# Optimization experiments

Measured on AMD Instinct MI355X. Metric: run time of the kernel, lower is better.

Reference implementation:

```python
import jax, jax.numpy as jnp
import numpy as np
from jax import lax

D_MODEL = 128
D_INNER = 256   # expand * d_model
D_STATE = 16
D_CONV = 4
DT_RANK = 8     # ceil(d_model / 16)
IN_CH = 64
SCALE = 0.02


def setup_inputs() -> dict:
    key = jax.random.key(0)
    ks = jax.random.split(key, 16)
    r = lambda k, s: jax.random.normal(k, s, dtype=jnp.float32)
    return {
        "x": r(ks[0], (4, IN_CH, 128, 128)),
        "conv_w": r(ks[1], (D_MODEL, IN_CH, 3, 3)) * SCALE,
        "conv_b": r(ks[2], (D_MODEL,)) * SCALE,
        "bn_g": jnp.ones((D_MODEL,), jnp.float32),
        "bn_b": jnp.zeros((D_MODEL,), jnp.float32),
        "bn_mean": r(ks[3], (D_MODEL,)) * SCALE,
        "bn_var": jax.random.uniform(ks[4], (D_MODEL,), jnp.float32) + 0.5,
        "in_w": r(ks[5], (2 * D_INNER, D_MODEL)) * SCALE,
        "conv1d_w": r(ks[6], (D_INNER, 1, D_CONV)) * SCALE,
        "conv1d_b": r(ks[7], (D_INNER,)) * SCALE,
        "xproj_w": r(ks[8], (DT_RANK + 2 * D_STATE, D_INNER)) * SCALE,
        "dtproj_w": r(ks[9], (D_INNER, DT_RANK)) * SCALE,
        "dtproj_b": r(ks[10], (D_INNER,)) * SCALE,
        "A_log": r(ks[11], (D_INNER, D_STATE)) * 0.5,
        "Dp": r(ks[12], (D_INNER,)) * SCALE,
        "out_w": r(ks[13], (D_MODEL, D_INNER)) * SCALE,
    }


def _mamba(u, in_w, conv1d_w, conv1d_b, xproj_w, dtproj_w, dtproj_b, A_log, Dp, out_w):
    # u: [B, L, d_model]
    xz = jnp.einsum("bld,ed->ble", u, in_w)          # [B, L, 2*d_inner]
    x_in, z = jnp.split(xz, 2, axis=-1)
    # depthwise causal conv1d over L
    xc = lax.conv_general_dilated(
        x_in.transpose(0, 2, 1), conv1d_w, (1,), [(D_CONV - 1, 0)],
        dimension_numbers=("NCL", "OIL", "NCL"), feature_group_count=D_INNER,
    ) + conv1d_b[None, :, None]
    x_in = jax.nn.silu(xc).transpose(0, 2, 1)         # [B, L, d_inner]

    x_dbl = jnp.einsum("bld,ed->ble", x_in, xproj_w)  # [B, L, dt_rank+2*d_state]
    dt, Bm, Cm = jnp.split(x_dbl, [DT_RANK, DT_RANK + D_STATE], axis=-1)
    delta = jax.nn.softplus(jnp.einsum("blr,dr->bld", dt, dtproj_w) + dtproj_b)

    A = -jnp.exp(A_log)                               # [d_inner, d_state]
    deltaA = jnp.exp(jnp.einsum("bld,dn->bldn", delta, A))        # [B,L,d,n]
    deltaBu = jnp.einsum("bld,bln,bld->bldn", delta, Bm, x_in)    # [B,L,d,n]

    def step(h, inp):
        dA, dBu, c = inp                              # [B,d,n],[B,d,n],[B,n]
        h = dA * h + dBu
        y = jnp.einsum("bdn,bn->bd", h, c)
        return h, y

    Bsz, L = u.shape[0], u.shape[1]
    h0 = jnp.zeros((Bsz, D_INNER, D_STATE), u.dtype)
    _, ys = lax.scan(step, h0, (deltaA.transpose(1, 0, 2, 3),
                                deltaBu.transpose(1, 0, 2, 3),
                                Cm.transpose(1, 0, 2)))
    y = ys.transpose(1, 0, 2) + x_in * Dp             # [B, L, d_inner]
    y = y * jax.nn.silu(z)
    return jnp.einsum("bld,ed->ble", y, out_w)        # [B, L, d_model]


def reference(x, conv_w, conv_b, bn_g, bn_b, bn_mean, bn_var, in_w, conv1d_w,
              conv1d_b, xproj_w, dtproj_w, dtproj_b, A_log, Dp, out_w):
    # downsample: conv3x3 stride2 + BN(eval) + exact GELU
    y = lax.conv_general_dilated(x, conv_w, (2, 2), [(1, 1), (1, 1)],
                                 dimension_numbers=("NCHW", "OIHW", "NCHW"))
    y = y + conv_b[None, :, None, None]
    inv = bn_g / jnp.sqrt(bn_var + 1e-5)
    y = (y - bn_mean[None, :, None, None]) * inv[None, :, None, None] + bn_b[None, :, None, None]
    y = jax.nn.gelu(y, approximate=False)             # [B, C, H, W]

    B, C, H, W = y.shape
    u = y.reshape(B, C, H * W).transpose(0, 2, 1)     # [B, L, C]
    out = _mamba(u, in_w, conv1d_w, conv1d_b, xproj_w, dtproj_w, dtproj_b,
                 A_log, Dp, out_w)
    out = out.transpose(0, 2, 1).reshape(B, C, H, W)
    return y + out
```

## Files before the change

kernel.cpp:

```cpp
#include <hip/hip_runtime.h>
#include <math.h>

#define NB 4
#define LTOK 4096
#define DM 128
#define DI 256
#define NCH 256
#define TCH 16
#define GSZ 16
#define NG  16

#define OFF_A2     0u
#define OFF_BIAS2  73728u
#define OFF_YDSR   84096u
#define OFF_XPRE   2181248u
#define OFF_S0     4278400u
#define OFF_Z      6375552u
#define OFF_DELTA  10569856u
#define OFF_S1     12667008u
#define OFF_BC     14764160u
#define OFF_DSUM   15288448u
#define OFF_GS     15550592u
#define OFF_GD     15812736u
#define OFF_XT     15829120u
#define OFF_WBF    17926272u
#define OFF_WCMP   17963136u
#define OFF_DPREF  18004096u
#define OFF_INWBF  19052672u
#define OFF_OUTWBF 19085440u

#define DEV __device__ __forceinline__
#define L2E 1.4426950408889634f

typedef short bh8 __attribute__((ext_vector_type(8)));
typedef float f4v __attribute__((ext_vector_type(4)));

DEV float fast_silu(float v) {
  return v * __builtin_amdgcn_rcpf(1.f + __expf(-v));
}

DEV unsigned short f2bf(float f) {
  unsigned int u = __float_as_uint(f);
  u = (u + 0x7FFFu + ((u >> 16) & 1u)) >> 16;
  return (unsigned short)u;
}

DEV float bf2f(unsigned short us) {
  return __uint_as_float((unsigned int)us << 16);
}

DEV float upk(const unsigned int* p, int i) {
  unsigned int u = p[i >> 1];
  return __uint_as_float((i & 1) ? (u & 0xFFFF0000u) : (u << 16));
}

__global__ __launch_bounds__(256) void k0x_prep(
    const float* __restrict__ conv_w, const float* __restrict__ conv_b,
    const float* __restrict__ bn_g, const float* __restrict__ bn_b,
    const float* __restrict__ bn_mean, const float* __restrict__ bn_var,
    const float* __restrict__ xproj_w, const float* __restrict__ A_log,
    const float* __restrict__ dtw, const float* __restrict__ in_w,
    const float* __restrict__ out_w, const float* __restrict__ x,
    float* __restrict__ ws) {
  __shared__ float t[64][65];
  if (blockIdx.x >= 1009) {
    const int bid = blockIdx.x - 1009;
    unsigned short* xt = (unsigned short*)(ws + OFF_XT);
    const int tid = threadIdx.x;
    const int ixh = bid & 1;
    const int iy = (bid >> 1) & 127;
    const int b = bid >> 8;
    {
      const int ixl = tid & 63, cw = tid >> 6;
#pragma unroll 4
      for (int i = 0; i < 16; ++i) {
        int ci = cw * 16 + i;
        t[ci][ixl] = x[(((size_t)(b * 64 + ci) * 128) + iy) * 128 + ixh * 64 + ixl];
      }
    }
    __syncthreads();
    {
      const int cil = tid & 63, iw = tid >> 6;
      unsigned short* dst = xt + (((size_t)(b * 128 + iy) * 128) + ixh * 64) * 64;
#pragma unroll 4
      for (int i = 0; i < 16; ++i) {
        int ix = iw * 16 + i;
        dst[ix * 64 + cil] = f2bf(t[cil][ix]);
      }
    }
    return;
  }
  int i = blockIdx.x * 256 + threadIdx.x;
  if (i < 73728) {
    int ci = i & 63; int tap = (i >> 6) % 9; int co = i / 576;
    float inv = bn_g[co] * rsqrtf(bn_var[co] + 1e-5f);
    ((unsigned short*)(ws + OFF_WBF))[i] = f2bf(conv_w[co * 576 + ci * 9 + tap] * inv);
  } else if (i < 73856) {
    int co = i - 73728;
    float inv = bn_g[co] * rsqrtf(bn_var[co] + 1e-5f);
    ws[OFF_BIAS2 + co] = (conv_b[co] - bn_mean[co]) * inv + bn_b[co];
  } else if (i < 77952) {
    int j = i - 73856;
    ws[OFF_A2 + j] = -__expf(A_log[j]) * L2E;
  } else if (i < 159872) {
    int j = i - 77952;
    int n = j >> 8, k = j & 255;
    float v = 0.f;
    if (n < 256) {
#pragma unroll
      for (int r = 0; r < 8; ++r)
        v = fmaf(dtw[n * 8 + r], xproj_w[r * 256 + k], v);
    } else if (n < 288) {
      v = xproj_w[(8 + n - 256) * 256 + k];
    }
    ((unsigned short*)(ws + OFF_WCMP))[j] = f2bf(v);
  } else if (i < 225408) {
    int j = i - 159872;
    ((unsigned short*)(ws + OFF_INWBF))[j] = f2bf(in_w[j]);
  } else if (i < 258176) {
    int j = i - 225408;
    ((unsigned short*)(ws + OFF_OUTWBF))[j] = f2bf(out_w[j]);
  }
}

__global__ __launch_bounds__(512) void k12_conv_inproj(
    const unsigned short* __restrict__ xt, const unsigned short* __restrict__ wbf,
    const float* __restrict__ bias2, const unsigned short* __restrict__ inwbf,
    unsigned short* __restrict__ ydsr, unsigned short* __restrict__ xpre,
    unsigned short* __restrict__ z) {
  __shared__ unsigned short ldt[64][136];
  const int tid = threadIdx.x;
  const int lane = tid & 63;
  const int w = tid >> 6;
  const int col = lane & 15, quad = lane >> 4;
  const int oy = blockIdx.x & 63;
  const int b = blockIdx.x >> 6;
  const int co_w = w * 16;
  const int iy0 = 2 * oy - 1;
  const bh8 bzero = {};

  f4v acc[4];
#pragma unroll
  for (int nt = 0; nt < 4; ++nt) acc[nt] = (f4v){0.f, 0.f, 0.f, 0.f};
  const unsigned short* ap = wbf + (size_t)(co_w + col) * 576;
  for (int tap = 0; tap < 9; ++tap) {
    const int kh = tap / 3, kw = tap - kh * 3;
    const int iy = iy0 + kh;
    const unsigned short* xrow = xt + (long)(b * 128 + iy) * 8192;
    const bool oky = (iy >= 0);
#pragma unroll
    for (int kc = 0; kc < 2; ++kc) {
      const int cib = kc * 32 + quad * 8;
      bh8 a0 = *(const bh8*)&ap[tap * 64 + cib];
#pragma unroll
      for (int nt = 0; nt < 4; ++nt) {
        const int ix = 2 * (nt * 16 + col) - 1 + kw;
        bh8 bv = *(const bh8*)&xrow[(long)ix * 64 + cib];
        if (!(oky && ix >= 0)) bv = bzero;
        acc[nt] = __builtin_amdgcn_mfma_f32_16x16x32_bf16(a0, bv, acc[nt], 0, 0, 0);
      }
    }
  }
#pragma unroll
  for (int nt = 0; nt < 4; ++nt) {
    const int tok = nt * 16 + col;
    const int swz = (tok & 15) << 3;
#pragma unroll
    for (int r = 0; r < 4; ++r) {
      const int co = co_w + quad * 4 + r;
      float v = acc[nt][r] + bias2[co];
      float g = 0.5f * v * (1.f + erff(v * 0.70710678118f));
      unsigned short gb = f2bf(g);
      ydsr[(((size_t)(b * 128 + co) * 64) + oy) * 64 + tok] = gb;
      ldt[tok][co ^ swz] = gb;
    }
  }
  __syncthreads();

  const size_t tglob0 = (size_t)(b * 4096 + oy * 64);
#pragma unroll
  for (int tt = 0; tt < 4; ++tt) {
    const int row = tt * 16 + col;
    const int swz = (row & 15) << 3;
    bh8 afrag[4];
#pragma unroll
    for (int kb = 0; kb < 4; ++kb)
      afrag[kb] = *(const bh8*)&ldt[row][(quad * 8 + kb * 32) ^ swz];
    f4v acc2[4];
#pragma unroll
    for (int j = 0; j < 4; ++j) acc2[j] = (f4v){0.f, 0.f, 0.f, 0.f};
#pragma unroll
    for (int kb = 0; kb < 4; ++kb) {
#pragma unroll
      for (int j = 0; j < 4; ++j) {
        const int e_row = (w * 4 + j) * 16 + col;
        bh8 bfrag = *(const bh8*)&inwbf[(size_t)e_row * 128 + quad * 8 + kb * 32];
        acc2[j] = __builtin_amdgcn_mfma_f32_16x16x32_bf16(afrag[kb], bfrag, acc2[j], 0, 0, 0);
      }
    }
#pragma unroll
    for (int j = 0; j < 4; ++j) {
      const int e = (w * 4 + j) * 16 + col;
#pragma unroll
      for (int r = 0; r < 4; ++r) {
        const size_t t = tglob0 + tt * 16 + quad * 4 + r;
        if (e < 256) xpre[t * 256 + e] = f2bf(acc2[j][r]);
        else z[t * 256 + e - 256] = f2bf(acc2[j][r]);
      }
    }
  }
}

__global__ __launch_bounds__(256) void k45_mfma(
    const unsigned short* __restrict__ wcomp, const float* __restrict__ dtb,
    const unsigned short* __restrict__ xpre, const float* __restrict__ cw1,
    const float* __restrict__ cb1, const float* __restrict__ a2tab,
    unsigned short* __restrict__ xinbf, unsigned short* __restrict__ delta,
    float* __restrict__ bc, float* __restrict__ dsum,
    float* __restrict__ S0, float* __restrict__ S1) {
  __shared__ unsigned short ld_xin[16][264];
  __shared__ unsigned short ld_delta[16][264];
  __shared__ float ld_bc[16][33];
  const int tid = threadIdx.x;
  const int lane = tid & 63;
  const int w = tid >> 6;
  const int col = lane & 15, quad = lane >> 4;
  const int tt = blockIdx.x & 255, b = blockIdx.x >> 8;
  const int t0 = tt * 16;

  {
    const int d = tid;
    float4 w4 = *(const float4*)&cw1[d * 4];
    float bias = cb1[d];
    float xw[19];
    const unsigned short* xp = xpre + ((size_t)(b * 4096 + t0 - 3)) * 256 + d;
    if (tt > 0) {
#pragma unroll
      for (int i = 0; i < 19; ++i) xw[i] = bf2f(xp[(size_t)i * 256]);
    } else {
#pragma unroll
      for (int i = 0; i < 19; ++i) {
        int t = t0 - 3 + i;
        xw[i] = (t >= 0) ? bf2f(xp[(size_t)i * 256]) : 0.f;
      }
    }
    unsigned short* dst = xinbf + ((size_t)(b * 4096 + t0)) * 256 + d;
#pragma unroll
    for (int i = 0; i < 16; ++i) {
      float o = bias + w4.x * xw[i] + w4.y * xw[i + 1] + w4.z * xw[i + 2] +
                w4.w * xw[i + 3];
      unsigned short us = f2bf(fast_silu(o));
      ld_xin[i][d] = us;
      dst[(size_t)i * 256] = us;
    }
  }
  __syncthreads();

  {
    bh8 afrag[8];
#pragma unroll
    for (int kb = 0; kb < 8; ++kb)
      afrag[kb] = *(const bh8*)&ld_xin[col][quad * 8 + kb * 32];
    f4v acc[5];
#pragma unroll
    for (int j = 0; j < 5; ++j) acc[j] = (f4v){0.f, 0.f, 0.f, 0.f};

    const int nt0 = w * 5;
    const unsigned short* wb = wcomp + (size_t)(nt0 * 16 + col) * 256 + quad * 8;
#pragma unroll
    for (int kb = 0; kb < 8; ++kb) {
#pragma unroll
      for (int j = 0; j < 5; ++j) {
        bh8 bfrag = *(const bh8*)&wb[(size_t)j * 4096 + kb * 32];
        acc[j] = __builtin_amdgcn_mfma_f32_16x16x32_bf16(afrag[kb], bfrag, acc[j], 0, 0, 0);
      }
    }
#pragma unroll
    for (int j = 0; j < 5; ++j) {
      const int n = (nt0 + j) * 16 + col;
      if (n < 256) {
        float bias = dtb[n];
#pragma unroll
        for (int r = 0; r < 4; ++r) {
          float s = acc[j][r] + bias;
          float dl = fmaxf(s, 0.f) + __logf(1.f + __expf(-fabsf(s)));
          ld_delta[quad * 4 + r][n] = f2bf(dl);
        }
      } else if (n < 288) {
#pragma unroll
        for (int r = 0; r < 4; ++r) ld_bc[quad * 4 + r][n - 256] = acc[j][r];
      }
    }
  }
  __syncthreads();

  {
    const int d = tid;
    float A2[16];
#pragma unroll
    for (int j = 0; j < 4; ++j) {
      float4 a = *(const float4*)&a2tab[d * 16 + j * 4];
      A2[4 * j + 0] = a.x; A2[4 * j + 1] = a.y;
      A2[4 * j + 2] = a.z; A2[4 * j + 3] = a.w;
    }
    float h[16];
#pragma unroll
    for (int n = 0; n < 16; ++n) h[n] = 0.f;
    float ds = 0.f;
#pragma unroll 4
    for (int i = 0; i < TCH; ++i) {
      float dl = bf2f(ld_delta[i][d]);
      float xv = bf2f(ld_xin[i][d]);
      ds += dl;
      float dlx = dl * xv;
#pragma unroll
      for (int n = 0; n < 16; ++n)
        h[n] = fmaf(exp2f(dl * A2[n]), h[n], dlx * ld_bc[i][n]);
    }
    dsum[((size_t)b * NCH + tt) * 256 + d] = ds;
    float* S = (b & 2) ? (S1 + (size_t)(b & 1) * 1048576)
                       : (S0 + (size_t)(b & 1) * 1048576);
    const size_t sbase = ((size_t)tt * 16) * 256 + d;
#pragma unroll
    for (int n = 0; n < 16; ++n) S[sbase + (size_t)n * 256] = h[n];
  }

#pragma unroll
  for (int it = 0; it < 4; ++it) {
    int idx = it * 256 + tid;
    int row = idx >> 6, d4 = (idx & 63) * 4;
    unsigned long long pk = *(const unsigned long long*)&ld_delta[row][d4];
    *(unsigned long long*)&delta[((size_t)(b * 4096 + t0 + row)) * 256 + d4] = pk;
  }
  if (tid < 128) {
    int row = tid >> 3, q = (tid & 7) * 4;
    float4 v = make_float4(ld_bc[row][q], ld_bc[row][q + 1],
                           ld_bc[row][q + 2], ld_bc[row][q + 3]);
    *(float4*)&bc[((size_t)(b * 4096 + t0 + row)) * 32 + q] = v;
  }
}

__global__ __launch_bounds__(256) void k5b1_group(
    float* __restrict__ S0, float* __restrict__ S1,
    const float* __restrict__ dsum, const float* __restrict__ a2tab,
    float* __restrict__ Gs, float* __restrict__ Gd,
    float* __restrict__ dpref) {
  const int d = threadIdx.x;
  const int n = blockIdx.x & 15, g = (blockIdx.x >> 4) & (NG - 1),
            b = blockIdx.x >> 8;
  float* S = (b & 2) ? (S1 + (size_t)(b & 1) * 1048576)
                     : (S0 + (size_t)(b & 1) * 1048576);
  const float A2 = a2tab[d * 16 + n];
  const size_t s0 = ((size_t)(g * GSZ) * 16 + n) * 256 + d;
  const size_t d0 = ((size_t)b * NCH + g * GSZ) * 256 + d;
  float sv[GSZ], dv[GSZ];
#pragma unroll
  for (int k = 0; k < GSZ; ++k) {
    sv[k] = S[s0 + (size_t)k * 4096];
    dv[k] = dsum[d0 + (size_t)k * 256];
  }
  float h = 0.f, cum = 0.f;
#pragma unroll
  for (int k = 0; k < GSZ; ++k) {
    S[s0 + (size_t)k * 4096] = h;
    if (n == 0) dpref[d0 + (size_t)k * 256] = cum;
    h = fmaf(exp2f(A2 * dv[k]), h, sv[k]);
    cum += dv[k];
  }
  Gs[((size_t)(b * NG + g) * 16 + n) * 256 + d] = h;
  if (n == 0) Gd[((size_t)b * NG + g) * 256 + d] = cum;
}

__global__ __launch_bounds__(256) void k56_fused(
    const unsigned short* __restrict__ xinbf, const float* __restrict__ bc,
    const unsigned short* __restrict__ delta, const unsigned short* __restrict__ z,
    const float* __restrict__ a2tab, const float* __restrict__ Dp,
    const float* __restrict__ dpref, const float* __restrict__ Gs,
    const float* __restrict__ Gd,
    const float* __restrict__ S0, const float* __restrict__ S1,
    const unsigned short* __restrict__ outwbf, const unsigned short* __restrict__ ydsr,
    float* __restrict__ out) {
  __shared__ __align__(16) float bct[TCH * 32];
  __shared__ __align__(16) unsigned short ld_y[16][264];
  __shared__ float ldo[16][132];
  const int tid = threadIdx.x;
  const int d = tid;
  const int c = blockIdx.x & (NCH - 1), b = blockIdx.x >> 8;
  const int t0 = c * TCH;
  {
    const float* src = bc + (size_t)(b * 4096 + t0) * 32;
    for (int i = tid; i < TCH * 32; i += 256) bct[i] = src[i];
  }
  float A2[16];
#pragma unroll
  for (int j = 0; j < 4; ++j) {
    float4 a = *(const float4*)&a2tab[d * 16 + j * 4];
    A2[4 * j + 0] = a.x; A2[4 * j + 1] = a.y;
    A2[4 * j + 2] = a.z; A2[4 * j + 3] = a.w;
  }
  const float Dpd = Dp[d];
  const int g = c >> 4;
  const float dp0 = dpref[((size_t)b * NCH + c) * 256 + d];

  const size_t base = (size_t)(b * 4096 + t0) * 256 + d;
  unsigned int dlp[8], xvp[8], zvp[8];
  {
    const unsigned short* pd = delta + base;
    const unsigned short* px = xinbf + base;
    const unsigned short* pz = z + base;
#pragma unroll
    for (int j = 0; j < 8; ++j) {
      dlp[j] = (unsigned int)pd[(size_t)(2 * j) * 256] |
               ((unsigned int)pd[(size_t)(2 * j + 1) * 256] << 16);
      xvp[j] = (unsigned int)px[(size_t)(2 * j) * 256] |
               ((unsigned int)px[(size_t)(2 * j + 1) * 256] << 16);
      zvp[j] = (unsigned int)pz[(size_t)(2 * j) * 256] |
               ((unsigned int)pz[(size_t)(2 * j + 1) * 256] << 16);
    }
  }
  const float* S = (b & 2) ? (S1 + (size_t)(b & 1) * 1048576)
                           : (S0 + (size_t)(b & 1) * 1048576);
  const size_t sbase = ((size_t)c * 16) * 256 + d;
  float sv[16];
#pragma unroll
  for (int n = 0; n < 16; ++n) sv[n] = S[sbase + (size_t)n * 256];

  float h[16];
#pragma unroll
  for (int n = 0; n < 16; ++n) h[n] = 0.f;
#pragma unroll
  for (int gp = 0; gp < NG - 1; ++gp) {
    if (gp < g) {
      const float gdv = Gd[((size_t)b * NG + gp) * 256 + d];
      const size_t gb0 = ((size_t)(b * NG + gp) * 16) * 256 + d;
#pragma unroll
      for (int n = 0; n < 16; ++n)
        h[n] = fmaf(exp2f(A2[n] * gdv), h[n], Gs[gb0 + (size_t)n * 256]);
    }
  }
#pragma unroll
  for (int n = 0; n < 16; ++n)
    h[n] = fmaf(exp2f(A2[n] * dp0), h[n], sv[n]);
  __syncthreads();
#pragma unroll
  for (int i = 0; i < TCH; ++i) {
    float dl = upk(dlp, i);
    float xv = upk(xvp, i);
    float zv = upk(zvp, i);
    float dlx = dl * xv;
    const float* r = &bct[i * 32];
    float y = 0.f;
#pragma unroll
    for (int n = 0; n < 16; ++n) {
      h[n] = fmaf(exp2f(dl * A2[n]), h[n], dlx * r[n]);
      y = fmaf(h[n], r[16 + n], y);
    }
    ld_y[i][d] = f2bf((y + xv * Dpd) * fast_silu(zv));
  }
  __syncthreads();

  const int lane = tid & 63;
  const int w = tid >> 6;
  const int col = lane & 15, quad = lane >> 4;
  const int oy = t0 >> 6, ox0 = t0 & 63;
  bh8 afrag[8];
#pragma unroll
  for (int kb = 0; kb < 8; ++kb)
    afrag[kb] = *(const bh8*)&ld_y[col][quad * 8 + kb * 32];
  f4v acc[2];
#pragma unroll
  for (int j = 0; j < 2; ++j) acc[j] = (f4v){0.f, 0.f, 0.f, 0.f};
  const int nt0 = w * 2;
  const unsigned short* wb = outwbf + (size_t)(nt0 * 16 + col) * 256 + quad * 8;
#pragma unroll
  for (int kb = 0; kb < 8; ++kb) {
#pragma unroll
    for (int j = 0; j < 2; ++j) {
      bh8 bfrag = *(const bh8*)&wb[(size_t)j * 4096 + kb * 32];
      acc[j] = __builtin_amdgcn_mfma_f32_16x16x32_bf16(afrag[kb], bfrag, acc[j], 0, 0, 0);
    }
  }
#pragma unroll
  for (int j = 0; j < 2; ++j)
#pragma unroll
    for (int r = 0; r < 4; ++r)
      ldo[quad * 4 + r][(nt0 + j) * 16 + col] = acc[j][r];
  __syncthreads();
  {
    const int cc = tid >> 1, half = tid & 1;
    size_t obase = (((size_t)(b * 128 + cc) * 64) + oy) * 64 + ox0 + half * 8;
    const unsigned short* rp = ydsr + obase;
    const int m0 = half * 8;
    float4 o0 = make_float4(ldo[m0 + 0][cc] + bf2f(rp[0]), ldo[m0 + 1][cc] + bf2f(rp[1]),
                            ldo[m0 + 2][cc] + bf2f(rp[2]), ldo[m0 + 3][cc] + bf2f(rp[3]));
    float4 o1 = make_float4(ldo[m0 + 4][cc] + bf2f(rp[4]), ldo[m0 + 5][cc] + bf2f(rp[5]),
                            ldo[m0 + 6][cc] + bf2f(rp[6]), ldo[m0 + 7][cc] + bf2f(rp[7]));
    *(float4*)&out[obase] = o0;
    *(float4*)&out[obase + 4] = o1;
  }
}

extern "C" void kernel_launch(void* const* d_in, const int* in_sizes, int n_in,
                              void* d_out, int out_size, void* d_ws, size_t ws_size,
                              hipStream_t stream) {
  (void)in_sizes; (void)n_in; (void)out_size; (void)ws_size;
  const float* x        = (const float*)d_in[0];
  const float* conv_w   = (const float*)d_in[1];
  const float* conv_b   = (const float*)d_in[2];
  const float* bn_g     = (const float*)d_in[3];
  const float* bn_b     = (const float*)d_in[4];
  const float* bn_mean  = (const float*)d_in[5];
  const float* bn_var   = (const float*)d_in[6];
  const float* in_w     = (const float*)d_in[7];
  const float* conv1d_w = (const float*)d_in[8];
  const float* conv1d_b = (const float*)d_in[9];
  const float* xproj_w  = (const float*)d_in[10];
  const float* dtproj_w = (const float*)d_in[11];
  const float* dtproj_b = (const float*)d_in[12];
  const float* A_log    = (const float*)d_in[13];
  const float* Dp       = (const float*)d_in[14];
  const float* out_w    = (const float*)d_in[15];
  float* ws = (float*)d_ws;
  float* out = (float*)d_out;

  k0x_prep<<<2033, 256, 0, stream>>>(conv_w, conv_b, bn_g, bn_b, bn_mean, bn_var,
                                     xproj_w, A_log, dtproj_w, in_w, out_w, x, ws);
  k12_conv_inproj<<<256, 512, 0, stream>>>(
      (const unsigned short*)(ws + OFF_XT),
      (const unsigned short*)(ws + OFF_WBF), ws + OFF_BIAS2,
      (const unsigned short*)(ws + OFF_INWBF),
      (unsigned short*)(ws + OFF_YDSR),
      (unsigned short*)(ws + OFF_XPRE),
      (unsigned short*)(ws + OFF_Z));
  k45_mfma<<<1024, 256, 0, stream>>>((const unsigned short*)(ws + OFF_WCMP),
                                     dtproj_b,
                                     (const unsigned short*)(ws + OFF_XPRE),
                                     conv1d_w, conv1d_b, ws + OFF_A2,
                                     (unsigned short*)(ws + OFF_XT),
                                     (unsigned short*)(ws + OFF_DELTA),
                                     ws + OFF_BC, ws + OFF_DSUM,
                                     ws + OFF_S0, ws + OFF_S1);
  k5b1_group<<<1024, 256, 0, stream>>>(ws + OFF_S0, ws + OFF_S1, ws + OFF_DSUM,
                                       ws + OFF_A2, ws + OFF_GS, ws + OFF_GD,
                                       ws + OFF_DPREF);
  k56_fused<<<1024, 256, 0, stream>>>((const unsigned short*)(ws + OFF_XT),
                                      ws + OFF_BC,
                                      (const unsigned short*)(ws + OFF_DELTA),
                                      (const unsigned short*)(ws + OFF_Z),
                                      ws + OFF_A2, Dp, ws + OFF_DPREF,
                                      ws + OFF_GS, ws + OFF_GD,
                                      ws + OFF_S0, ws + OFF_S1,
                                      (const unsigned short*)(ws + OFF_OUTWBF),
                                      (const unsigned short*)(ws + OFF_YDSR), out);
}
```

Measured before the change: 219.3 us.

## Split scan state dimension across thread pairs in fused scan kernel

The fused scan/output kernel now uses 512 threads per block, with two threads per channel each owning 8 of the 16 state elements. The partial y dot products are combined with a lane shuffle, and the output MFMA and store stages are redistributed over 8 waves. The intent is to shorten the per-thread serial exp/FMA chain and cut register pressure for better latency hiding. The cost is redundant loads of delta/x/z per thread pair, an extra shuffle per timestep, and larger blocks.

```diff
diff --git a/kernel.cpp b/kernel.cpp
--- a/kernel.cpp
+++ b/kernel.cpp
@@ -371,7 +371,7 @@
   if (n == 0) Gd[((size_t)b * NG + g) * 256 + d] = cum;
 }
 
-__global__ __launch_bounds__(256) void k56_fused(
+__global__ __launch_bounds__(512) void k56_fused(
     const unsigned short* __restrict__ xinbf, const float* __restrict__ bc,
     const unsigned short* __restrict__ delta, const unsigned short* __restrict__ z,
     const float* __restrict__ a2tab, const float* __restrict__ Dp,
@@ -384,17 +384,19 @@
   __shared__ __align__(16) unsigned short ld_y[16][264];
   __shared__ float ldo[16][132];
   const int tid = threadIdx.x;
-  const int d = tid;
+  const int nh = tid & 1;
+  const int d = tid >> 1;
+  const int n0 = nh * 8;
   const int c = blockIdx.x & (NCH - 1), b = blockIdx.x >> 8;
   const int t0 = c * TCH;
   {
     const float* src = bc + (size_t)(b * 4096 + t0) * 32;
-    for (int i = tid; i < TCH * 32; i += 256) bct[i] = src[i];
-  }
-  float A2[16];
-#pragma unroll
-  for (int j = 0; j < 4; ++j) {
-    float4 a = *(const float4*)&a2tab[d * 16 + j * 4];
+    if (tid < TCH * 32) bct[tid] = src[tid];
+  }
+  float A2[8];
+#pragma unroll
+  for (int j = 0; j < 2; ++j) {
+    float4 a = *(const float4*)&a2tab[d * 16 + n0 + j * 4];
     A2[4 * j + 0] = a.x; A2[4 * j + 1] = a.y;
     A2[4 * j + 2] = a.z; A2[4 * j + 3] = a.w;
   }
@@ -420,26 +422,26 @@
   }
   const float* S = (b & 2) ? (S1 + (size_t)(b & 1) * 1048576)
                            : (S0 + (size_t)(b & 1) * 1048576);
-  const size_t sbase = ((size_t)c * 16) * 256 + d;
-  float sv[16];
-#pragma unroll
-  for (int n = 0; n < 16; ++n) sv[n] = S[sbase + (size_t)n * 256];
-
-  float h[16];
-#pragma unroll
-  for (int n = 0; n < 16; ++n) h[n] = 0.f;
+  const size_t sbase = ((size_t)c * 16 + n0) * 256 + d;
+  float sv[8];
+#pragma unroll
+  for (int n = 0; n < 8; ++n) sv[n] = S[sbase + (size_t)n * 256];
+
+  float h[8];
+#pragma unroll
+  for (int n = 0; n < 8; ++n) h[n] = 0.f;
 #pragma unroll
   for (int gp = 0; gp < NG - 1; ++gp) {
     if (gp < g) {
       const float gdv = Gd[((size_t)b * NG + gp) * 256 + d];
-      const size_t gb0 = ((size_t)(b * NG + gp) * 16) * 256 + d;
-#pragma unroll
-      for (int n = 0; n < 16; ++n)
+      const size_t gb0 = ((size_t)(b * NG + gp) * 16 + n0) * 256 + d;
+#pragma unroll
+      for (int n = 0; n < 8; ++n)
         h[n] = fmaf(exp2f(A2[n] * gdv), h[n], Gs[gb0 + (size_t)n * 256]);
     }
   }
 #pragma unroll
-  for (int n = 0; n < 16; ++n)
+  for (int n = 0; n < 8; ++n)
     h[n] = fmaf(exp2f(A2[n] * dp0), h[n], sv[n]);
   __syncthreads();
 #pragma unroll
@@ -448,14 +450,16 @@
     float xv = upk(xvp, i);
     float zv = upk(zvp, i);
     float dlx = dl * xv;
-    const float* r = &bct[i * 32];
-    float y = 0.f;
-#pragma unroll
-    for (int n = 0; n < 16; ++n) {
+    const float* r = &bct[i * 32 + n0];
+    float yp = 0.f;
+#pragma unroll
+    for (int n = 0; n < 8; ++n) {
       h[n] = fmaf(exp2f(dl * A2[n]), h[n], dlx * r[n]);
-      y = fmaf(h[n], r[16 + n], y);
-    }
-    ld_y[i][d] = f2bf((y + xv * Dpd) * fast_silu(zv));
+      yp = fmaf(h[n], r[16 + n], yp);
+    }
+    float y = yp + __shfl_xor(yp, 1);
+    if (nh == 0)
+      ld_y[i][d] = f2bf((y + xv * Dpd) * fast_silu(zv));
   }
   __syncthreads();
 
@@ -467,36 +471,25 @@
 #pragma unroll
   for (int kb = 0; kb < 8; ++kb)
     afrag[kb] = *(const bh8*)&ld_y[col][quad * 8 + kb * 32];
-  f4v acc[2];
-#pragma unroll
-  for (int j = 0; j < 2; ++j) acc[j] = (f4v){0.f, 0.f, 0.f, 0.f};
-  const int nt0 = w * 2;
-  const unsigned short* wb = outwbf + (size_t)(nt0 * 16 + col) * 256 + quad * 8;
+  f4v acc = (f4v){0.f, 0.f, 0.f, 0.f};
+  const unsigned short* wb = outwbf + (size_t)(w * 16 + col) * 256 + quad * 8;
 #pragma unroll
   for (int kb = 0; kb < 8; ++kb) {
-#pragma unroll
-    for (int j = 0; j < 2; ++j) {
-      bh8 bfrag = *(const bh8*)&wb[(size_t)j * 4096 + kb * 32];
-      acc[j] = __builtin_amdgcn_mfma_f32_16x16x32_bf16(afrag[kb], bfrag, acc[j], 0, 0, 0);
-    }
-  }
-#pragma unroll
-  for (int j = 0; j < 2; ++j)
-#pragma unroll
-    for (int r = 0; r < 4; ++r)
-      ldo[quad * 4 + r][(nt0 + j) * 16 + col] = acc[j][r];
+    bh8 bfrag = *(const bh8*)&wb[kb * 32];
+    acc = __builtin_amdgcn_mfma_f32_16x16x32_bf16(afrag[kb], bfrag, acc, 0, 0, 0);
+  }
+#pragma unroll
+  for (int r = 0; r < 4; ++r)
+    ldo[quad * 4 + r][w * 16 + col] = acc[r];
   __syncthreads();
   {
-    const int cc = tid >> 1, half = tid & 1;
-    size_t obase = (((size_t)(b * 128 + cc) * 64) + oy) * 64 + ox0 + half * 8;
+    const int cc = tid >> 2, q = tid & 3;
+    size_t obase = (((size_t)(b * 128 + cc) * 64) + oy) * 64 + ox0 + q * 4;
     const unsigned short* rp = ydsr + obase;
-    const int m0 = half * 8;
+    const int m0 = q * 4;
     float4 o0 = make_float4(ldo[m0 + 0][cc] + bf2f(rp[0]), ldo[m0 + 1][cc] + bf2f(rp[1]),
                             ldo[m0 + 2][cc] + bf2f(rp[2]), ldo[m0 + 3][cc] + bf2f(rp[3]));
-    float4 o1 = make_float4(ldo[m0 + 4][cc] + bf2f(rp[4]), ldo[m0 + 5][cc] + bf2f(rp[5]),
-                            ldo[m0 + 6][cc] + bf2f(rp[6]), ldo[m0 + 7][cc] + bf2f(rp[7]));
     *(float4*)&out[obase] = o0;
-    *(float4*)&out[obase + 4] = o1;
   }
 }
 
@@ -543,7 +536,7 @@
   k5b1_group<<<1024, 256, 0, stream>>>(ws + OFF_S0, ws + OFF_S1, ws + OFF_DSUM,
                                        ws + OFF_A2, ws + OFF_GS, ws + OFF_GD,
                                        ws + OFF_DPREF);
-  k56_fused<<<1024, 256, 0, stream>>>((const unsigned short*)(ws + OFF_XT),
+  k56_fused<<<1024, 512, 0, stream>>>((const unsigned short*)(ws + OFF_XT),
                                       ws + OFF_BC,
                                       (const unsigned short*)(ws + OFF_DELTA),
                                       (const unsigned short*)(ws + OFF_Z),
```

Result: slower. 226.2 us (+3.2%).

## Add group-prefix scan kernel and process two chunks per block with LDS staging

Applied to the files above, without the earlier changes.

Moves the inter-group state prefix computation, previously redone by every block in a serial loop over up to 15 groups, into a new small kernel that writes exclusive group prefixes into Gs. The fused scan and out-projection kernel now handles 32 tokens per block instead of 16, halving the grid. It stages delta, x and z through LDS with coalesced uint4 loads rather than strided 2-byte loads, and runs the out-projection MFMA in two 16-row passes. This removes redundant exp2 work and uncoalesced reads, at the cost of an extra launch, a longer serial scan per block, more LDS use, and fewer blocks in flight.

```diff
diff --git a/kernel.cpp b/kernel.cpp
--- a/kernel.cpp
+++ b/kernel.cpp
@@ -47,11 +47,6 @@
 
 DEV float bf2f(unsigned short us) {
   return __uint_as_float((unsigned int)us << 16);
-}
-
-DEV float upk(const unsigned int* p, int i) {
-  unsigned int u = p[i >> 1];
-  return __uint_as_float((i & 1) ? (u & 0xFFFF0000u) : (u << 16));
 }
 
 __global__ __launch_bounds__(256) void k0x_prep(
@@ -371,26 +366,68 @@
   if (n == 0) Gd[((size_t)b * NG + g) * 256 + d] = cum;
 }
 
+__global__ __launch_bounds__(256) void k5b2_groupscan(
+    float* __restrict__ Gs, const float* __restrict__ Gd,
+    const float* __restrict__ a2tab) {
+  const int d = threadIdx.x;
+  const int n = blockIdx.x & 15, b = blockIdx.x >> 4;
+  const float A2 = a2tab[d * 16 + n];
+  float sv[NG], dv[NG];
+  const size_t g0 = ((size_t)(b * NG) * 16 + n) * 256 + d;
+  const size_t gd0 = (size_t)b * NG * 256 + d;
+#pragma unroll
+  for (int g = 0; g < NG; ++g) {
+    sv[g] = Gs[g0 + (size_t)g * 4096];
+    dv[g] = Gd[gd0 + (size_t)g * 256];
+  }
+  float h = 0.f;
+#pragma unroll
+  for (int g = 0; g < NG; ++g) {
+    Gs[g0 + (size_t)g * 4096] = h;
+    h = fmaf(exp2f(A2 * dv[g]), h, sv[g]);
+  }
+}
+
 __global__ __launch_bounds__(256) void k56_fused(
     const unsigned short* __restrict__ xinbf, const float* __restrict__ bc,
     const unsigned short* __restrict__ delta, const unsigned short* __restrict__ z,
     const float* __restrict__ a2tab, const float* __restrict__ Dp,
     const float* __restrict__ dpref, const float* __restrict__ Gs,
-    const float* __restrict__ Gd,
     const float* __restrict__ S0, const float* __restrict__ S1,
     const unsigned short* __restrict__ outwbf, const unsigned short* __restrict__ ydsr,
     float* __restrict__ out) {
-  __shared__ __align__(16) float bct[TCH * 32];
-  __shared__ __align__(16) unsigned short ld_y[16][264];
+  __shared__ __align__(16) float bct[32 * 32];
+  __shared__ __align__(16) unsigned short sdd[32][264];
+  __shared__ __align__(16) unsigned short sdx[32][264];
+  __shared__ __align__(16) unsigned short sdz[32][264];
   __shared__ float ldo[16][132];
   const int tid = threadIdx.x;
   const int d = tid;
-  const int c = blockIdx.x & (NCH - 1), b = blockIdx.x >> 8;
-  const int t0 = c * TCH;
+  const int cp = blockIdx.x & 127, b = blockIdx.x >> 7;
+  const int c0 = cp * 2;
+  const int t0 = cp * 32;
+  const size_t gbase = (size_t)(b * 4096 + t0) * 256;
+
   {
-    const float* src = bc + (size_t)(b * 4096 + t0) * 32;
-    for (int i = tid; i < TCH * 32; i += 256) bct[i] = src[i];
-  }
+    const uint4* gd = (const uint4*)(delta + gbase);
+    const uint4* gx = (const uint4*)(xinbf + gbase);
+    const uint4* gz = (const uint4*)(z + gbase);
+#pragma unroll
+    for (int k = 0; k < 4; ++k) {
+      const int idx = k * 256 + tid;
+      const int row = idx >> 5, c4 = idx & 31;
+      uint4 vd = gd[idx];
+      uint4 vx = gx[idx];
+      uint4 vz = gz[idx];
+      *(uint4*)&sdd[row][c4 * 8] = vd;
+      *(uint4*)&sdx[row][c4 * 8] = vx;
+      *(uint4*)&sdz[row][c4 * 8] = vz;
+    }
+    const float* srcbc = bc + (size_t)(b * 4096 + t0) * 32;
+#pragma unroll
+    for (int k = 0; k < 4; ++k) bct[k * 256 + tid] = srcbc[k * 256 + tid];
+  }
+
   float A2[16];
 #pragma unroll
   for (int j = 0; j < 4; ++j) {
@@ -399,54 +436,26 @@
     A2[4 * j + 2] = a.z; A2[4 * j + 3] = a.w;
   }
   const float Dpd = Dp[d];
-  const int g = c >> 4;
-  const float dp0 = dpref[((size_t)b * NCH + c) * 256 + d];
-
-  const size_t base = (size_t)(b * 4096 + t0) * 256 + d;
-  unsigned int dlp[8], xvp[8], zvp[8];
-  {
-    const unsigned short* pd = delta + base;
-    const unsigned short* px = xinbf + base;
-    const unsigned short* pz = z + base;
-#pragma unroll
-    for (int j = 0; j < 8; ++j) {
-      dlp[j] = (unsigned int)pd[(size_t)(2 * j) * 256] |
-               ((unsigned int)pd[(size_t)(2 * j + 1) * 256] << 16);
-      xvp[j] = (unsigned int)px[(size_t)(2 * j) * 256] |
-               ((unsigned int)px[(size_t)(2 * j + 1) * 256] << 16);
-      zvp[j] = (unsigned int)pz[(size_t)(2 * j) * 256] |
-               ((unsigned int)pz[(size_t)(2 * j + 1) * 256] << 16);
-    }
-  }
+  const int g = c0 >> 4;
+  const float dp0 = dpref[((size_t)b * NCH + c0) * 256 + d];
   const float* S = (b & 2) ? (S1 + (size_t)(b & 1) * 1048576)
                            : (S0 + (size_t)(b & 1) * 1048576);
-  const size_t sbase = ((size_t)c * 16) * 256 + d;
-  float sv[16];
-#pragma unroll
-  for (int n = 0; n < 16; ++n) sv[n] = S[sbase + (size_t)n * 256];
-
+  const size_t sbase = ((size_t)c0 * 16) * 256 + d;
+  const size_t gsb = ((size_t)(b * NG + g) * 16) * 256 + d;
   float h[16];
 #pragma unroll
-  for (int n = 0; n < 16; ++n) h[n] = 0.f;
-#pragma unroll
-  for (int gp = 0; gp < NG - 1; ++gp) {
-    if (gp < g) {
-      const float gdv = Gd[((size_t)b * NG + gp) * 256 + d];
-      const size_t gb0 = ((size_t)(b * NG + gp) * 16) * 256 + d;
-#pragma unroll
-      for (int n = 0; n < 16; ++n)
-        h[n] = fmaf(exp2f(A2[n] * gdv), h[n], Gs[gb0 + (size_t)n * 256]);
-    }
-  }
-#pragma unroll
-  for (int n = 0; n < 16; ++n)
-    h[n] = fmaf(exp2f(A2[n] * dp0), h[n], sv[n]);
+  for (int n = 0; n < 16; ++n) {
+    float gi = Gs[gsb + (size_t)n * 256];
+    float hl = S[sbase + (size_t)n * 256];
+    h[n] = fmaf(exp2f(A2[n] * dp0), gi, hl);
+  }
   __syncthreads();
-#pragma unroll
-  for (int i = 0; i < TCH; ++i) {
-    float dl = upk(dlp, i);
-    float xv = upk(xvp, i);
-    float zv = upk(zvp, i);
+
+#pragma unroll
+  for (int i = 0; i < 32; ++i) {
+    float dl = bf2f(sdd[i][d]);
+    float xv = bf2f(sdx[i][d]);
+    float zv = bf2f(sdz[i][d]);
     float dlx = dl * xv;
     const float* r = &bct[i * 32];
     float y = 0.f;
@@ -455,7 +464,7 @@
       h[n] = fmaf(exp2f(dl * A2[n]), h[n], dlx * r[n]);
       y = fmaf(h[n], r[16 + n], y);
     }
-    ld_y[i][d] = f2bf((y + xv * Dpd) * fast_silu(zv));
+    sdz[i][d] = f2bf((y + xv * Dpd) * fast_silu(zv));
   }
   __syncthreads();
 
@@ -463,40 +472,44 @@
   const int w = tid >> 6;
   const int col = lane & 15, quad = lane >> 4;
   const int oy = t0 >> 6, ox0 = t0 & 63;
-  bh8 afrag[8];
-#pragma unroll
-  for (int kb = 0; kb < 8; ++kb)
-    afrag[kb] = *(const bh8*)&ld_y[col][quad * 8 + kb * 32];
-  f4v acc[2];
-#pragma unroll
-  for (int j = 0; j < 2; ++j) acc[j] = (f4v){0.f, 0.f, 0.f, 0.f};
-  const int nt0 = w * 2;
-  const unsigned short* wb = outwbf + (size_t)(nt0 * 16 + col) * 256 + quad * 8;
-#pragma unroll
-  for (int kb = 0; kb < 8; ++kb) {
-#pragma unroll
-    for (int j = 0; j < 2; ++j) {
-      bh8 bfrag = *(const bh8*)&wb[(size_t)j * 4096 + kb * 32];
-      acc[j] = __builtin_amdgcn_mfma_f32_16x16x32_bf16(afrag[kb], bfrag, acc[j], 0, 0, 0);
-    }
-  }
-#pragma unroll
-  for (int j = 0; j < 2; ++j)
-#pragma unroll
-    for (int r = 0; r < 4; ++r)
-      ldo[quad * 4 + r][(nt0 + j) * 16 + col] = acc[j][r];
-  __syncthreads();
-  {
-    const int cc = tid >> 1, half = tid & 1;
-    size_t obase = (((size_t)(b * 128 + cc) * 64) + oy) * 64 + ox0 + half * 8;
-    const unsigned short* rp = ydsr + obase;
-    const int m0 = half * 8;
-    float4 o0 = make_float4(ldo[m0 + 0][cc] + bf2f(rp[0]), ldo[m0 + 1][cc] + bf2f(rp[1]),
-                            ldo[m0 + 2][cc] + bf2f(rp[2]), ldo[m0 + 3][cc] + bf2f(rp[3]));
-    float4 o1 = make_float4(ldo[m0 + 4][cc] + bf2f(rp[4]), ldo[m0 + 5][cc] + bf2f(rp[5]),
-                            ldo[m0 + 6][cc] + bf2f(rp[6]), ldo[m0 + 7][cc] + bf2f(rp[7]));
-    *(float4*)&out[obase] = o0;
-    *(float4*)&out[obase + 4] = o1;
+#pragma unroll
+  for (int tt = 0; tt < 2; ++tt) {
+    bh8 afrag[8];
+#pragma unroll
+    for (int kb = 0; kb < 8; ++kb)
+      afrag[kb] = *(const bh8*)&sdz[tt * 16 + col][quad * 8 + kb * 32];
+    f4v acc[2];
+#pragma unroll
+    for (int j = 0; j < 2; ++j) acc[j] = (f4v){0.f, 0.f, 0.f, 0.f};
+    const int nt0 = w * 2;
+    const unsigned short* wb = outwbf + (size_t)(nt0 * 16 + col) * 256 + quad * 8;
+#pragma unroll
+    for (int kb = 0; kb < 8; ++kb) {
+#pragma unroll
+      for (int j = 0; j < 2; ++j) {
+        bh8 bfrag = *(const bh8*)&wb[(size_t)j * 4096 + kb * 32];
+        acc[j] = __builtin_amdgcn_mfma_f32_16x16x32_bf16(afrag[kb], bfrag, acc[j], 0, 0, 0);
+      }
+    }
+#pragma unroll
+    for (int j = 0; j < 2; ++j)
+#pragma unroll
+      for (int r = 0; r < 4; ++r)
+        ldo[quad * 4 + r][(nt0 + j) * 16 + col] = acc[j][r];
+    __syncthreads();
+    {
+      const int cc = tid >> 1, half = tid & 1;
+      size_t obase = (((size_t)(b * 128 + cc) * 64) + oy) * 64 + ox0 + tt * 16 + half * 8;
+      const unsigned short* rp = ydsr + obase;
+      const int m0 = half * 8;
+      float4 o0 = make_float4(ldo[m0 + 0][cc] + bf2f(rp[0]), ldo[m0 + 1][cc] + bf2f(rp[1]),
+                              ldo[m0 + 2][cc] + bf2f(rp[2]), ldo[m0 + 3][cc] + bf2f(rp[3]));
+      float4 o1 = make_float4(ldo[m0 + 4][cc] + bf2f(rp[4]), ldo[m0 + 5][cc] + bf2f(rp[5]),
+                              ldo[m0 + 6][cc] + bf2f(rp[6]), ldo[m0 + 7][cc] + bf2f(rp[7]));
+      *(float4*)&out[obase] = o0;
+      *(float4*)&out[obase + 4] = o1;
+    }
+    __syncthreads();
   }
 }
 
@@ -543,13 +556,14 @@
   k5b1_group<<<1024, 256, 0, stream>>>(ws + OFF_S0, ws + OFF_S1, ws + OFF_DSUM,
                                        ws + OFF_A2, ws + OFF_GS, ws + OFF_GD,
                                        ws + OFF_DPREF);
-  k56_fused<<<1024, 256, 0, stream>>>((const unsigned short*)(ws + OFF_XT),
-                                      ws + OFF_BC,
-                                      (const unsigned short*)(ws + OFF_DELTA),
-                                      (const unsigned short*)(ws + OFF_Z),
-                                      ws + OFF_A2, Dp, ws + OFF_DPREF,
-                                      ws + OFF_GS, ws + OFF_GD,
-                                      ws + OFF_S0, ws + OFF_S1,
-                                      (const unsigned short*)(ws + OFF_OUTWBF),
-                                      (const unsigned short*)(ws + OFF_YDSR), out);
-}
+  k5b2_groupscan<<<64, 256, 0, stream>>>(ws + OFF_GS, ws + OFF_GD, ws + OFF_A2);
+  k56_fused<<<512, 256, 0, stream>>>((const unsigned short*)(ws + OFF_XT),
+                                     ws + OFF_BC,
+                                     (const unsigned short*)(ws + OFF_DELTA),
+                                     (const unsigned short*)(ws + OFF_Z),
+                                     ws + OFF_A2, Dp, ws + OFF_DPREF,
+                                     ws + OFF_GS,
+                                     ws + OFF_S0, ws + OFF_S1,
+                                     (const unsigned short*)(ws + OFF_OUTWBF),
+                                     (const unsigned short*)(ws + OFF_YDSR), out);
+}
```

New measurement: 207.8 us, median of 3. 5.2% less time.
